# Kernel optimization log

Measured on AMD Instinct MI355X. Metric: run time of the kernel, lower is better.

## Reference

```python
import jax, jax.numpy as jnp
import numpy as np


def setup_inputs() -> dict:
    key = jax.random.key(0)
    kq, kk, kv = jax.random.split(key, 3)
    B, T, S, A = 32, 1024, 1024, 512
    queries = jax.random.normal(kq, (B, T, A), dtype=jnp.float32)
    keys = jax.random.normal(kk, (B, S, A), dtype=jnp.float32)
    values = jax.random.normal(kv, (B, S, A), dtype=jnp.float32)
    attn_mask = jnp.zeros((B, T, S), dtype=jnp.float32)  # additive mask
    return {"queries": queries, "keys": keys, "values": values, "attn_mask": attn_mask}


def reference(queries, keys, values, attn_mask):
    # score(): scaled dot-product, the canonical concrete scoring fn
    A = queries.shape[-1]
    scale = 1.0 / jnp.sqrt(jnp.asarray(A, dtype=queries.dtype))
    weights = jnp.einsum("bta,bsa->bts", queries, keys) * scale  # [B,T,S]
    weights = weights + attn_mask  # additive mask
    weights = jax.nn.softmax(weights, axis=-1)
    out = jnp.einsum("bts,bsa->bta", weights, values)  # [B,T,A]
    return out
```

## Files before the change

### kernel.cpp

```cpp
#include <hip/hip_runtime.h>

typedef __attribute__((ext_vector_type(8))) short short8;
typedef __attribute__((ext_vector_type(4))) float f32x4;

#define B_  32
#define T_  1024
#define S_  1024
#define A_  512
#define SCALE_ 0.044194173824159216f
#define L2E_ 1.4426950408889634f

__device__ __forceinline__ unsigned short f2bf(float f) {
    unsigned int u = __float_as_uint(f);
    u += 0x7fffu + ((u >> 16) & 1u);
    return (unsigned short)(u >> 16);
}
__device__ __forceinline__ unsigned int pack2(float lo, float hi) {
    return (unsigned int)f2bf(lo) | ((unsigned int)f2bf(hi) << 16);
}

__global__ __launch_bounds__(256)
void prep_k(const float* __restrict__ K, unsigned char* __restrict__ Kws) {
    const int gid = blockIdx.x * 256 + threadIdx.x;
    const int u = gid & 63;
    const int r = gid >> 6;
    const int s = r & 31;
    const float* src = K + (size_t)r * A_ + u * 8;
    float4 x = *(const float4*)src;
    float4 y = *(const float4*)(src + 4);
    uint4 w;
    w.x = pack2(x.x, x.y); w.y = pack2(x.z, x.w);
    w.z = pack2(y.x, y.y); w.w = pack2(y.z, y.w);
    *(uint4*)(Kws + (size_t)(r >> 5) * 32768 + s * 1024 + ((u ^ (s & 7)) << 4)) = w;
}

__global__ __launch_bounds__(256)
void prep_v(const float* __restrict__ V, unsigned char* __restrict__ Vws) {
    const int tile = blockIdx.x >> 1;
    const int a = ((blockIdx.x & 1) << 8) + threadIdx.x;
    const float* src = V + (size_t)tile * 32 * A_ + a;
    float col[32];
    #pragma unroll
    for (int s = 0; s < 32; ++s) col[s] = src[(size_t)s * A_];
    unsigned int w[16];
    #pragma unroll
    for (int j = 0; j < 16; ++j) w[j] = pack2(col[2 * j], col[2 * j + 1]);
    unsigned char* dst = Vws + (size_t)tile * 32768 + a * 64;
    #pragma unroll
    for (int q = 0; q < 4; ++q) {
        uint4 o; o.x = w[q*4]; o.y = w[q*4+1]; o.z = w[q*4+2]; o.w = w[q*4+3];
        *(uint4*)(dst + q * 16) = o;
    }
}

__global__ __launch_bounds__(512, 2)
void attn_fwd_ws(const float* __restrict__ Qg, const unsigned char* __restrict__ Kws,
                 const unsigned char* __restrict__ Vws, const float* __restrict__ Mg,
                 float* __restrict__ Og)
{
    __shared__ unsigned char lds[141312];
    const int tid  = threadIdx.x;
    const int wave = tid >> 6;
    const int lane = tid & 63;
    const int l15  = lane & 15;
    const int lg   = lane >> 4;

    const int bid = blockIdx.x;
    const int xcd = bid & 7, idx = bid >> 3;
    const int b  = xcd * 4 + (idx >> 3);
    const int rb = idx & 7;
    const int qb = rb * 128 + wave * 16;

    const float* Qb = Qg + (size_t)b * T_ * A_;
    const float* Mb = Mg + (size_t)b * T_ * S_;
    float*       Ob = Og + (size_t)b * T_ * A_;
    const unsigned char* Kbase = Kws + (size_t)b * 32 * 32768;
    const unsigned char* Vbase = Vws + (size_t)b * 32 * 32768;

    short8 qf[16];
    {
        const float* qrow = Qb + (size_t)(qb + l15) * A_ + lg * 8;
        #pragma unroll
        for (int c = 0; c < 16; ++c) {
            float4 x = *(const float4*)(qrow + c * 32);
            float4 y = *(const float4*)(qrow + c * 32 + 4);
            union { short8 s; unsigned int u[4]; } t;
            t.u[0] = pack2(x.x, x.y); t.u[1] = pack2(x.z, x.w);
            t.u[2] = pack2(y.x, y.y); t.u[3] = pack2(y.z, y.w);
            qf[c] = t.s;
        }
    }

    const f32x4 fz = {};
    f32x4 oacc[32];
    #pragma unroll
    for (int at = 0; at < 32; ++at) oacc[at] = fz;
    float m_run[4], l_run[4];
    #pragma unroll
    for (int r = 0; r < 4; ++r) { m_run[r] = -1e30f; l_run[r] = 0.0f; }

    const int s7r = l15 & 7;

    #define STAGE(bsel, st)                                                        \
    {                                                                              \
        const unsigned char* kg = Kbase + (size_t)(st) * 32768;                    \
        const unsigned char* vg = Vbase + (size_t)(st) * 32768;                    \
        _Pragma("unroll")                                                          \
        for (int c = 0; c < 4; ++c) {                                              \
            const int o = (wave + c * 8) * 1024;                                   \
            __builtin_amdgcn_global_load_lds(                                      \
                (const __attribute__((address_space(1))) void*)(kg + o + lane*16), \
                (__attribute__((address_space(3))) void*)(lds + (bsel)*32768 + o), \
                16, 0, 0);                                                         \
            __builtin_amdgcn_global_load_lds(                                      \
                (const __attribute__((address_space(1))) void*)(vg + o + lane*16), \
                (__attribute__((address_space(3))) void*)(lds + 65536 + (bsel)*32768 + o), \
                16, 0, 0);                                                         \
        }                                                                          \
    }

    STAGE(0, 0);
    int cur = 0;

    for (int kt = 0; kt < 32; ++kt) {
        __builtin_amdgcn_s_barrier();
        __builtin_amdgcn_sched_barrier(0);
        float mk0[4], mk1[4];
        {
            const float* mrow = Mb + (size_t)(qb + lg * 4) * S_ + kt * 32 + l15;
            #pragma unroll
            for (int r = 0; r < 4; ++r) {
                mk0[r] = mrow[(size_t)r * S_];
                mk1[r] = mrow[(size_t)r * S_ + 16];
            }
        }
        __builtin_amdgcn_sched_barrier(0);
        const int sidx = (kt + 1 < 32) ? kt + 1 : 31;
        STAGE(cur ^ 1, sidx);
        asm volatile("s_waitcnt vmcnt(16)");
        __builtin_amdgcn_sched_barrier(0);
        __builtin_amdgcn_s_barrier();
        __builtin_amdgcn_sched_barrier(0);

        f32x4 acc0 = fz, acc1 = fz;
        const unsigned char* Kl = lds + cur * 32768;
        #pragma unroll
        for (int c = 0; c < 16; ++c) {
            const int u = c * 4 + lg;
            short8 b0 = *(const short8*)(Kl + l15 * 1024 + ((u ^ s7r) << 4));
            short8 b1 = *(const short8*)(Kl + (l15 + 16) * 1024 + ((u ^ s7r) << 4));
            acc0 = __builtin_amdgcn_mfma_f32_16x16x32_bf16(qf[c], b0, acc0, 0, 0, 0);
            acc1 = __builtin_amdgcn_mfma_f32_16x16x32_bf16(qf[c], b1, acc1, 0, 0, 0);
        }

        float sc0[4], sc1[4], mt[4];
        #pragma unroll
        for (int r = 0; r < 4; ++r) {
            sc0[r] = acc0[r] * SCALE_ + mk0[r];
            sc1[r] = acc1[r] * SCALE_ + mk1[r];
            mt[r]  = fmaxf(sc0[r], sc1[r]);
        }
        #pragma unroll
        for (int off = 1; off < 16; off <<= 1) {
            #pragma unroll
            for (int r = 0; r < 4; ++r)
                mt[r] = fmaxf(mt[r], __shfl_xor(mt[r], off));
        }
        bool need = false;
        #pragma unroll
        for (int r = 0; r < 4; ++r) need = need || (mt[r] > m_run[r] + 8.0f);
        if (__any(need)) {
            #pragma unroll
            for (int r = 0; r < 4; ++r) {
                const float mn = fmaxf(m_run[r], mt[r]);
                const float al = exp2f((m_run[r] - mn) * L2E_);
                l_run[r] *= al;
                m_run[r] = mn;
                #pragma unroll
                for (int at = 0; at < 32; ++at) oacc[at][r] *= al;
            }
        }
        float p0[4], p1[4], lsum[4];
        #pragma unroll
        for (int r = 0; r < 4; ++r) {
            p0[r] = exp2f((sc0[r] - m_run[r]) * L2E_);
            p1[r] = exp2f((sc1[r] - m_run[r]) * L2E_);
            lsum[r] = p0[r] + p1[r];
        }
        #pragma unroll
        for (int off = 1; off < 16; off <<= 1) {
            #pragma unroll
            for (int r = 0; r < 4; ++r)
                lsum[r] += __shfl_xor(lsum[r], off);
        }
        #pragma unroll
        for (int r = 0; r < 4; ++r) l_run[r] += lsum[r];

        unsigned char* pl = lds + 131072 + wave * 1280;
        #pragma unroll
        for (int r = 0; r < 4; ++r) {
            const int row = lg * 4 + r;
            *(unsigned short*)(pl + row * 80 + l15 * 2)        = f2bf(p0[r]);
            *(unsigned short*)(pl + row * 80 + (l15 + 16) * 2) = f2bf(p1[r]);
        }
        short8 pa = *(const short8*)(pl + l15 * 80 + lg * 16);

        const unsigned char* Vl = lds + 65536 + cur * 32768;
        #pragma unroll
        for (int at = 0; at < 32; ++at) {
            short8 vb = *(const short8*)(Vl + (at * 16 + l15) * 64 + lg * 16);
            oacc[at] = __builtin_amdgcn_mfma_f32_16x16x32_bf16(pa, vb, oacc[at], 0, 0, 0);
        }
        cur ^= 1;
    }
    asm volatile("s_waitcnt vmcnt(0)");

    #pragma unroll
    for (int r = 0; r < 4; ++r) {
        const float inv = 1.0f / l_run[r];
        float* orow = Ob + (size_t)(qb + lg * 4 + r) * A_ + l15;
        #pragma unroll
        for (int at = 0; at < 32; ++at)
            orow[at * 16] = oacc[at][r] * inv;
    }
    #undef STAGE
}

__global__ __launch_bounds__(256, 2)
void attn_fwd_fb(const float* __restrict__ Qg, const float* __restrict__ Kg,
                 const float* __restrict__ Vg, const float* __restrict__ Mg,
                 float* __restrict__ Og)
{
    __shared__ unsigned char lds[65536];
    const int tid  = threadIdx.x;
    const int wave = tid >> 6;
    const int lane = tid & 63;
    const int l15  = lane & 15;
    const int lg   = lane >> 4;
    const int i    = blockIdx.x;
    const int slot = i >> 3;
    const int b    = (i & 7) * 4 + (slot >> 4);
    const int qb   = (slot & 15) * 64 + wave * 16;

    const float* Qb = Qg + (size_t)b * T_ * A_;
    const float* Kb = Kg + (size_t)b * S_ * A_;
    const float* Vb = Vg + (size_t)b * S_ * A_;
    const float* Mb = Mg + (size_t)b * T_ * S_;
    float*       Ob = Og + (size_t)b * T_ * A_;

    short8 qf[16];
    {
        const float* qrow = Qb + (size_t)(qb + l15) * A_ + lg * 8;
        #pragma unroll
        for (int c = 0; c < 16; ++c) {
            float4 x = *(const float4*)(qrow + c * 32);
            float4 y = *(const float4*)(qrow + c * 32 + 4);
            union { short8 s; unsigned int u[4]; } t;
            t.u[0] = pack2(x.x, x.y); t.u[1] = pack2(x.z, x.w);
            t.u[2] = pack2(y.x, y.y); t.u[3] = pack2(y.z, y.w);
            qf[c] = t.s;
        }
    }
    const f32x4 fz = {};
    f32x4 oacc[32];
    #pragma unroll
    for (int at = 0; at < 32; ++at) oacc[at] = fz;
    float m_run[4], l_run[4];
    #pragma unroll
    for (int r = 0; r < 4; ++r) { m_run[r] = -1e30f; l_run[r] = 0.0f; }

    const int ks  = tid >> 3;
    const int kcb = tid & 7;
    const int ks7 = ks & 7;
    const int vsp = tid & 15;
    const int vac = tid >> 4;
    const int vs0 = vsp * 2;
    const int vu  = vs0 >> 3;
    const int vco = (vs0 & 7) * 2;
    const int s7r  = l15 & 7;
    const int vswz = (lg ^ (l15 & 3)) << 4;

    for (int kt = 0; kt < 32; ++kt) {
        const int kb = kt * 32;
        __syncthreads();
        {
            const float* krow = Kb + (size_t)(kb + ks) * A_ + kcb * 8;
            unsigned char* kdst = lds + ks * 1024;
            #pragma unroll
            for (int jj = 0; jj < 8; ++jj) {
                float4 x = *(const float4*)(krow + jj * 64);
                float4 y = *(const float4*)(krow + jj * 64 + 4);
                uint4 w;
                w.x = pack2(x.x, x.y); w.y = pack2(x.z, x.w);
                w.z = pack2(y.x, y.y); w.w = pack2(y.z, y.w);
                const int u = kcb + jj * 8;
                *(uint4*)(kdst + ((u ^ ks7) << 4)) = w;
            }
        }
        {
            const float* v0 = Vb + (size_t)(kb + vs0) * A_ + vac * 4;
            const float* v1 = v0 + A_;
            #pragma unroll
            for (int jj = 0; jj < 8; ++jj) {
                float4 x = *(const float4*)(v0 + jj * 64);
                float4 y = *(const float4*)(v1 + jj * 64);
                const int a0 = vac * 4 + jj * 64;
                float xs[4] = {x.x, x.y, x.z, x.w};
                float ys[4] = {y.x, y.y, y.z, y.w};
                #pragma unroll
                for (int ii = 0; ii < 4; ++ii) {
                    const int a = a0 + ii;
                    *(unsigned int*)(lds + 32768 + a * 64 + ((vu ^ (a & 3)) << 4) + vco)
                        = pack2(xs[ii], ys[ii]);
                }
            }
        }
        float mk0[4], mk1[4];
        {
            const float* mrow = Mb + (size_t)(qb + lg * 4) * S_ + kb + l15;
            #pragma unroll
            for (int r = 0; r < 4; ++r) {
                mk0[r] = mrow[(size_t)r * S_];
                mk1[r] = mrow[(size_t)r * S_ + 16];
            }
        }
        __syncthreads();
        f32x4 acc0 = fz, acc1 = fz;
        #pragma unroll
        for (int c = 0; c < 16; ++c) {
            const int u = c * 4 + lg;
            short8 b0 = *(const short8*)(lds + l15 * 1024 + ((u ^ s7r) << 4));
            short8 b1 = *(const short8*)(lds + (l15 + 16) * 1024 + ((u ^ s7r) << 4));
            acc0 = __builtin_amdgcn_mfma_f32_16x16x32_bf16(qf[c], b0, acc0, 0, 0, 0);
            acc1 = __builtin_amdgcn_mfma_f32_16x16x32_bf16(qf[c], b1, acc1, 0, 0, 0);
        }
        float sc0[4], sc1[4], mt[4];
        #pragma unroll
        for (int r = 0; r < 4; ++r) {
            sc0[r] = acc0[r] * SCALE_ + mk0[r];
            sc1[r] = acc1[r] * SCALE_ + mk1[r];
            mt[r]  = fmaxf(sc0[r], sc1[r]);
        }
        #pragma unroll
        for (int off = 1; off < 16; off <<= 1) {
            #pragma unroll
            for (int r = 0; r < 4; ++r)
                mt[r] = fmaxf(mt[r], __shfl_xor(mt[r], off));
        }
        bool need = false;
        #pragma unroll
        for (int r = 0; r < 4; ++r) need = need || (mt[r] > m_run[r] + 8.0f);
        if (__any(need)) {
            #pragma unroll
            for (int r = 0; r < 4; ++r) {
                const float mn = fmaxf(m_run[r], mt[r]);
                const float al = exp2f((m_run[r] - mn) * L2E_);
                l_run[r] *= al;
                m_run[r] = mn;
                #pragma unroll
                for (int at = 0; at < 32; ++at) oacc[at][r] *= al;
            }
        }
        float p0[4], p1[4], lsum[4];
        #pragma unroll
        for (int r = 0; r < 4; ++r) {
            p0[r] = exp2f((sc0[r] - m_run[r]) * L2E_);
            p1[r] = exp2f((sc1[r] - m_run[r]) * L2E_);
            lsum[r] = p0[r] + p1[r];
        }
        #pragma unroll
        for (int off = 1; off < 16; off <<= 1) {
            #pragma unroll
            for (int r = 0; r < 4; ++r)
                lsum[r] += __shfl_xor(lsum[r], off);
        }
        #pragma unroll
        for (int r = 0; r < 4; ++r) l_run[r] += lsum[r];
        __syncthreads();
        unsigned char* pl = lds + wave * 1280;
        #pragma unroll
        for (int r = 0; r < 4; ++r) {
            const int row = lg * 4 + r;
            *(unsigned short*)(pl + row * 80 + l15 * 2)        = f2bf(p0[r]);
            *(unsigned short*)(pl + row * 80 + (l15 + 16) * 2) = f2bf(p1[r]);
        }
        short8 pa = *(const short8*)(pl + l15 * 80 + lg * 16);
        #pragma unroll
        for (int at = 0; at < 32; ++at) {
            short8 vb = *(const short8*)(lds + 32768 + (at * 16 + l15) * 64 + vswz);
            oacc[at] = __builtin_amdgcn_mfma_f32_16x16x32_bf16(pa, vb, oacc[at], 0, 0, 0);
        }
    }
    #pragma unroll
    for (int r = 0; r < 4; ++r) {
        const float inv = 1.0f / l_run[r];
        float* orow = Ob + (size_t)(qb + lg * 4 + r) * A_ + l15;
        #pragma unroll
        for (int at = 0; at < 32; ++at)
            orow[at * 16] = oacc[at][r] * inv;
    }
}

extern "C" void kernel_launch(void* const* d_in, const int* in_sizes, int n_in,
                              void* d_out, int out_size, void* d_ws, size_t ws_size,
                              hipStream_t stream) {
    const float* Q = (const float*)d_in[0];
    const float* K = (const float*)d_in[1];
    const float* V = (const float*)d_in[2];
    const float* M = (const float*)d_in[3];
    float* O = (float*)d_out;
    const size_t need = (size_t)64 * 1024 * 1024;
    if (ws_size >= need) {
        unsigned char* Kws = (unsigned char*)d_ws;
        unsigned char* Vws = Kws + (size_t)32 * 1024 * 1024;
        prep_k<<<dim3(8192), dim3(256), 0, stream>>>(K, Kws);
        prep_v<<<dim3(2048), dim3(256), 0, stream>>>(V, Vws);
        attn_fwd_ws<<<dim3(256), dim3(512), 0, stream>>>(Q, Kws, Vws, M, O);
    } else {
        attn_fwd_fb<<<dim3(512), dim3(256), 0, stream>>>(Q, K, V, M, O);
    }
}
```

Measured before the change: 195.7 us.

## Shrink attention blocks to 4 waves and single-buffer K/V with staggered prefetch

The main attention kernel now runs 512 blocks of 256 threads, each covering 64 query rows, instead of 256 blocks of 512 threads covering 128 rows. This halves LDS use (about 69 KB) so that two blocks can fit per CU. K and V now use single buffers. The V tile is loaded while QK^T runs, and the next K tile is loaded while softmax and PV run, with extra barriers and vmcnt waits in between. MFMA sections are raised with s_setprio. The intent is more resident blocks and better latency hiding, but the change adds synchronisation and a full vmcnt(0) drain every iteration, and K/V tiles are reloaded twice as often across blocks.

```diff
diff --git a/kernel.cpp b/kernel.cpp
--- a/kernel.cpp
+++ b/kernel.cpp
@@ -53,12 +53,12 @@
     }
 }
 
-__global__ __launch_bounds__(512, 2)
+__global__ __launch_bounds__(256, 2)
 void attn_fwd_ws(const float* __restrict__ Qg, const unsigned char* __restrict__ Kws,
                  const unsigned char* __restrict__ Vws, const float* __restrict__ Mg,
                  float* __restrict__ Og)
 {
-    __shared__ unsigned char lds[141312];
+    __shared__ unsigned char lds[70656];
     const int tid  = threadIdx.x;
     const int wave = tid >> 6;
     const int lane = tid & 63;
@@ -67,9 +67,9 @@
 
     const int bid = blockIdx.x;
     const int xcd = bid & 7, idx = bid >> 3;
-    const int b  = xcd * 4 + (idx >> 3);
-    const int rb = idx & 7;
-    const int qb = rb * 128 + wave * 16;
+    const int b   = xcd * 4 + (idx >> 4);
+    const int rb  = idx & 15;
+    const int qb  = rb * 64 + wave * 16;
 
     const float* Qb = Qg + (size_t)b * T_ * A_;
     const float* Mb = Mg + (size_t)b * T_ * S_;
@@ -101,30 +101,26 @@
 
     const int s7r = l15 & 7;
 
-    #define STAGE(bsel, st)                                                        \
+    #define STAGE8(gsrc, ldsoff)                                                   \
     {                                                                              \
-        const unsigned char* kg = Kbase + (size_t)(st) * 32768;                    \
-        const unsigned char* vg = Vbase + (size_t)(st) * 32768;                    \
         _Pragma("unroll")                                                          \
-        for (int c = 0; c < 4; ++c) {                                              \
-            const int o = (wave + c * 8) * 1024;                                   \
+        for (int c = 0; c < 8; ++c) {                                              \
+            const int o = c * 4096 + wave * 1024;                                  \
             __builtin_amdgcn_global_load_lds(                                      \
-                (const __attribute__((address_space(1))) void*)(kg + o + lane*16), \
-                (__attribute__((address_space(3))) void*)(lds + (bsel)*32768 + o), \
-                16, 0, 0);                                                         \
-            __builtin_amdgcn_global_load_lds(                                      \
-                (const __attribute__((address_space(1))) void*)(vg + o + lane*16), \
-                (__attribute__((address_space(3))) void*)(lds + 65536 + (bsel)*32768 + o), \
+                (const __attribute__((address_space(1))) void*)((gsrc) + o + lane*16), \
+                (__attribute__((address_space(3))) void*)(lds + (ldsoff) + o),     \
                 16, 0, 0);                                                         \
         }                                                                          \
     }
 
-    STAGE(0, 0);
-    int cur = 0;
+    STAGE8(Kbase, 0);
+    asm volatile("s_waitcnt vmcnt(0)");
+    __builtin_amdgcn_sched_barrier(0);
 
     for (int kt = 0; kt < 32; ++kt) {
         __builtin_amdgcn_s_barrier();
         __builtin_amdgcn_sched_barrier(0);
+
         float mk0[4], mk1[4];
         {
             const float* mrow = Mb + (size_t)(qb + lg * 4) * S_ + kt * 32 + l15;
@@ -135,23 +131,28 @@
             }
         }
         __builtin_amdgcn_sched_barrier(0);
-        const int sidx = (kt + 1 < 32) ? kt + 1 : 31;
-        STAGE(cur ^ 1, sidx);
-        asm volatile("s_waitcnt vmcnt(16)");
-        __builtin_amdgcn_sched_barrier(0);
-        __builtin_amdgcn_s_barrier();
+        STAGE8(Vbase + (size_t)kt * 32768, 32768);
         __builtin_amdgcn_sched_barrier(0);
 
         f32x4 acc0 = fz, acc1 = fz;
-        const unsigned char* Kl = lds + cur * 32768;
+        __builtin_amdgcn_s_setprio(1);
         #pragma unroll
         for (int c = 0; c < 16; ++c) {
             const int u = c * 4 + lg;
-            short8 b0 = *(const short8*)(Kl + l15 * 1024 + ((u ^ s7r) << 4));
-            short8 b1 = *(const short8*)(Kl + (l15 + 16) * 1024 + ((u ^ s7r) << 4));
+            short8 b0 = *(const short8*)(lds + l15 * 1024 + ((u ^ s7r) << 4));
+            short8 b1 = *(const short8*)(lds + (l15 + 16) * 1024 + ((u ^ s7r) << 4));
             acc0 = __builtin_amdgcn_mfma_f32_16x16x32_bf16(qf[c], b0, acc0, 0, 0, 0);
             acc1 = __builtin_amdgcn_mfma_f32_16x16x32_bf16(qf[c], b1, acc1, 0, 0, 0);
         }
+        __builtin_amdgcn_s_setprio(0);
+        __builtin_amdgcn_sched_barrier(0);
+        __builtin_amdgcn_s_barrier();
+        __builtin_amdgcn_sched_barrier(0);
+        {
+            const int sidx = (kt + 1 < 32) ? kt + 1 : 31;
+            STAGE8(Kbase + (size_t)sidx * 32768, 0);
+        }
+        __builtin_amdgcn_sched_barrier(0);
 
         float sc0[4], sc1[4], mt[4];
         #pragma unroll
@@ -196,7 +197,7 @@
         #pragma unroll
         for (int r = 0; r < 4; ++r) l_run[r] += lsum[r];
 
-        unsigned char* pl = lds + 131072 + wave * 1280;
+        unsigned char* pl = lds + 65536 + wave * 1280;
         #pragma unroll
         for (int r = 0; r < 4; ++r) {
             const int row = lg * 4 + r;
@@ -205,15 +206,22 @@
         }
         short8 pa = *(const short8*)(pl + l15 * 80 + lg * 16);
 
-        const unsigned char* Vl = lds + 65536 + cur * 32768;
+        asm volatile("s_waitcnt vmcnt(8)");
+        __builtin_amdgcn_sched_barrier(0);
+        __builtin_amdgcn_s_barrier();
+        __builtin_amdgcn_sched_barrier(0);
+
+        __builtin_amdgcn_s_setprio(1);
         #pragma unroll
         for (int at = 0; at < 32; ++at) {
-            short8 vb = *(const short8*)(Vl + (at * 16 + l15) * 64 + lg * 16);
+            short8 vb = *(const short8*)(lds + 32768 + (at * 16 + l15) * 64 + lg * 16);
             oacc[at] = __builtin_amdgcn_mfma_f32_16x16x32_bf16(pa, vb, oacc[at], 0, 0, 0);
         }
-        cur ^= 1;
-    }
-    asm volatile("s_waitcnt vmcnt(0)");
+        __builtin_amdgcn_s_setprio(0);
+        __builtin_amdgcn_sched_barrier(0);
+        asm volatile("s_waitcnt vmcnt(0)");
+        __builtin_amdgcn_sched_barrier(0);
+    }
 
     #pragma unroll
     for (int r = 0; r < 4; ++r) {
@@ -223,7 +231,7 @@
         for (int at = 0; at < 32; ++at)
             orow[at * 16] = oacc[at][r] * inv;
     }
-    #undef STAGE
+    #undef STAGE8
 }
 
 __global__ __launch_bounds__(256, 2)
@@ -415,7 +423,7 @@
         unsigned char* Vws = Kws + (size_t)32 * 1024 * 1024;
         prep_k<<<dim3(8192), dim3(256), 0, stream>>>(K, Kws);
         prep_v<<<dim3(2048), dim3(256), 0, stream>>>(V, Vws);
-        attn_fwd_ws<<<dim3(256), dim3(512), 0, stream>>>(Q, Kws, Vws, M, O);
+        attn_fwd_ws<<<dim3(512), dim3(256), 0, stream>>>(Q, Kws, Vws, M, O);
     } else {
         attn_fwd_fb<<<dim3(512), dim3(256), 0, stream>>>(Q, K, V, M, O);
     }
```

After: 744.9 us. 281% more time.
